# Optimization experiments

Measured on AMD Instinct MI355X. Metric: run time of the kernel, lower is better.

Reference implementation:

```python
import jax, jax.numpy as jnp
import numpy as np

EPS = 1e-5

def _offset_conv(x, w, b):
    # 3x3 conv, padding=1, producing 2*K*K offset channels (standard DeformConv2D v1)
    out = jax.lax.conv_general_dilated(x, w, (1, 1), ((1, 1), (1, 1)),
                                       dimension_numbers=('NCHW', 'OIHW', 'NCHW'))
    return out + b[None, :, None, None]

def _bilinear_gather(x, py, px):
    # x: [B,C,H,W]; py,px: [B,K2,H,W] float sample coords -> [B,C,K2,H,W]
    B, C, H, W = x.shape
    py = jnp.clip(py, 0.0, H - 1.0)
    px = jnp.clip(px, 0.0, W - 1.0)
    y0 = jnp.floor(py)
    x0 = jnp.floor(px)
    wy = py - y0
    wx = px - x0
    y0i = y0.astype(jnp.int32)
    x0i = x0.astype(jnp.int32)
    y1i = jnp.minimum(y0i + 1, H - 1)
    x1i = jnp.minimum(x0i + 1, W - 1)
    xf = x.reshape(B, C, H * W)
    K2, Ho, Wo = py.shape[1], py.shape[2], py.shape[3]
    def gather(yy, xx):
        idx = (yy * W + xx).reshape(B, 1, -1)  # broadcast over C
        return jnp.take_along_axis(xf, idx, axis=2).reshape(B, C, K2, Ho, Wo)
    v00 = gather(y0i, x0i)
    v01 = gather(y0i, x1i)
    v10 = gather(y1i, x0i)
    v11 = gather(y1i, x1i)
    wy = wy[:, None]
    wx = wx[:, None]
    return (v00 * (1 - wy) * (1 - wx) + v01 * (1 - wy) * wx
            + v10 * wy * (1 - wx) + v11 * wy * wx)

def _deform_dw(x, w_off, b_off, w_dw, k):
    # depthwise deformable conv, kernel k, padding k//2 (same spatial size)
    B, C, H, W = x.shape
    K2 = k * k
    off = _offset_conv(x, w_off, b_off)      # [B, 2*K2, H, W]
    dy, dx = off[:, :K2], off[:, K2:]
    r = (k - 1) // 2
    pn = jnp.arange(-r, r + 1, dtype=x.dtype)
    pn_y = jnp.repeat(pn, k)[None, :, None, None]  # [1,K2,1,1]
    pn_x = jnp.tile(pn, k)[None, :, None, None]
    gy = jnp.arange(H, dtype=x.dtype)[None, None, :, None]
    gx = jnp.arange(W, dtype=x.dtype)[None, None, None, :]
    py = gy + pn_y + dy
    px = gx + pn_x + dx
    samp = _bilinear_gather(x, py, px)        # [B,C,K2,H,W]
    return jnp.einsum('bckhw,ck->bchw', samp, w_dw.reshape(C, K2))

def _bn_relu(x, g, b, m, v):
    inv = g / jnp.sqrt(v + EPS)
    return jax.nn.relu(x * inv[None, :, None, None] + (b - m * inv)[None, :, None, None])

def setup_inputs() -> dict:
    key = jax.random.key(0)
    B, C, H, W, O = 4, 96, 64, 64, 192
    ks = jax.random.split(key, 32)
    d = {'x': jax.random.normal(ks[0], (B, C, H, W), jnp.float32)}
    i = 1
    for k in (3, 5, 7):
        K2 = k * k
        d[f'w_off{k}'] = 0.01 * jax.random.normal(ks[i], (2 * K2, C, 3, 3), jnp.float32); i += 1
        d[f'b_off{k}'] = jnp.zeros((2 * K2,), jnp.float32)
        d[f'w_dw{k}'] = jax.random.normal(ks[i], (C, k, k), jnp.float32) / k; i += 1
        d[f'g{k}'] = jnp.ones((C,), jnp.float32)
        d[f'be{k}'] = jnp.zeros((C,), jnp.float32)
        d[f'm{k}'] = 0.1 * jax.random.normal(ks[i], (C,), jnp.float32); i += 1
        d[f'v{k}'] = jax.random.uniform(ks[i], (C,), jnp.float32, 0.5, 1.5); i += 1
    d['w_pw'] = jax.random.normal(ks[i], (O, 3 * C), jnp.float32) / np.sqrt(3 * C).astype(np.float32); i += 1
    d['gp'] = jnp.ones((O,), jnp.float32)
    d['bp'] = jnp.zeros((O,), jnp.float32)
    d['mp'] = 0.1 * jax.random.normal(ks[i], (O,), jnp.float32); i += 1
    d['vp'] = jax.random.uniform(ks[i], (O,), jnp.float32, 0.5, 1.5)
    return d

def reference(x, w_off3, b_off3, w_dw3, g3, be3, m3, v3,
              w_off5, b_off5, w_dw5, g5, be5, m5, v5,
              w_off7, b_off7, w_dw7, g7, be7, m7, v7,
              w_pw, gp, bp, mp, vp):
    x1 = _bn_relu(_deform_dw(x, w_off3, b_off3, w_dw3, 3), g3, be3, m3, v3)
    x2 = _bn_relu(_deform_dw(x, w_off5, b_off5, w_dw5, 5), g5, be5, m5, v5)
    x3 = _bn_relu(_deform_dw(x, w_off7, b_off7, w_dw7, 7), g7, be7, m7, v7)
    xc = jnp.concatenate([x1, x2, x3], axis=1)  # [B, 3C, H, W]
    out = jnp.einsum('bchw,oc->bohw', xc, w_pw)  # 1x1 conv
    return _bn_relu(out, gp, bp, mp, vp)
```

## Files before the change

kernel.cpp:

```cpp
#include <hip/hip_runtime.h>
#include <hip/hip_fp16.h>
#include <math.h>

typedef unsigned short u16;
typedef _Float16 f16x8 __attribute__((ext_vector_type(8)));
typedef float f32x4 __attribute__((ext_vector_type(4)));

#define HWp 4096
#define Cc 96
#define Bb 4
#define Oo 192
#define C3 288

#define OFF_WDWT  0
#define OFF_BCAT  14112
#define OFF_SBR   14304
#define OFF_HBR   14592
#define OFF_SPW   14880
#define OFF_HPW   15072
#define FP32_END  15264
#define BF_XTPAD  0
#define BF_WOF    1672704
#define BF_WPW    1838592

__device__ __forceinline__ u16 f2h(float f) { return __half_as_ushort(__float2half(f)); }
__device__ __forceinline__ unsigned h2u(__half2 h) { union { __half2 h; unsigned u; } t; t.h = h; return t.u; }
__device__ __forceinline__ __half2 u2h(unsigned u) { union { __half2 h; unsigned u; } t; t.u = u; return t.h; }

#define PREP_N (165888 + 55296 + 14112 + 192 + 288 + 288 + 192 + 192 + 24960)
#define PREP_BLK ((PREP_N + 255) / 256)

__global__ __launch_bounds__(256) void prep_kernel(
    const float* __restrict__ x,
    const float* __restrict__ w3, const float* __restrict__ b3, const float* __restrict__ dw3,
    const float* __restrict__ g3, const float* __restrict__ be3, const float* __restrict__ m3, const float* __restrict__ v3,
    const float* __restrict__ w5, const float* __restrict__ b5, const float* __restrict__ dw5,
    const float* __restrict__ g5, const float* __restrict__ be5, const float* __restrict__ m5, const float* __restrict__ v5,
    const float* __restrict__ w7, const float* __restrict__ b7, const float* __restrict__ dw7,
    const float* __restrict__ g7, const float* __restrict__ be7, const float* __restrict__ m7, const float* __restrict__ v7,
    const float* __restrict__ wpw,
    const float* __restrict__ gp, const float* __restrict__ bp, const float* __restrict__ mp, const float* __restrict__ vp,
    float* __restrict__ ws)
{
    __shared__ u16 sT[64 * 104];
    u16* bf = (u16*)(ws + FP32_END);
    const int tid = threadIdx.x;

    if (blockIdx.x < 256) {
        const int b = blockIdx.x >> 6, h = blockIdx.x & 63;
        const float* xb = x + (((size_t)b * Cc) << 12) + (h << 6);
#pragma unroll
        for (int it = 0; it < 24; ++it) {
            int j = tid + it * 256;
            int c = j >> 6, p = j & 63;
            sT[p * 104 + c] = f2h(xb[((size_t)c << 12) + p]);
        }
        __syncthreads();
        u16* dst = bf + BF_XTPAD + ((size_t)(b * 66 + h + 1) * 66 + 1) * 96;
#pragma unroll
        for (int it = 0; it < 6; ++it) {
            int j = tid + it * 256;
            int pos = j / 24, c4 = j % 24;
            const u16* s = &sT[pos * 104 + c4 * 4];
            *(uint2*)(dst + pos * 96 + c4 * 4) = make_uint2(
                (unsigned)s[0] | ((unsigned)s[1] << 16),
                (unsigned)s[2] | ((unsigned)s[3] << 16));
        }
        return;
    }

    int i = (blockIdx.x - 256) * 256 + tid;
    if (i < 165888) {
        int f = i / 13824, r = i % 13824;
        int s = r >> 9, l = r & 511;
        int lane = l >> 3, j = l & 7;
        int o = f * 16 + (lane & 15);
        int k = s * 32 + (lane >> 4) * 8 + j;
        int tap = k / 96, c = k % 96;
        float v = 0.f;
        if (o < 18)       v = w3[o * 864 + c * 9 + tap];
        else if (o < 68)  v = w5[(o - 18) * 864 + c * 9 + tap];
        else if (o < 166) v = w7[(o - 68) * 864 + c * 9 + tap];
        bf[BF_WOF + i] = f2h(v);
        return;
    }
    int j = i - 165888;
    if (j < 55296) {
        int f = j / 4608, r = j % 4608;
        int s = r >> 9, l = r & 511;
        int lane = l >> 3, jj = l & 7;
        int o = f * 16 + (lane & 15);
        int k = s * 32 + (lane >> 4) * 8 + jj;
        bf[BF_WPW + j] = f2h(wpw[o * C3 + k]);
        return;
    }
    j -= 55296;
    if (j < 14112) {
        int ksel = j / 4704, rem = j % 4704;
        int t = rem / 96, c = rem % 96;
        int K2 = (ksel == 0) ? 9 : (ksel == 1) ? 25 : 49;
        const float* dw = (ksel == 0) ? dw3 : (ksel == 1) ? dw5 : dw7;
        ws[OFF_WDWT + j] = (t < K2) ? dw[c * K2 + t] : 0.f;
        return;
    }
    j -= 14112;
    if (j < 192) {
        float v = 0.f;
        if (j < 18)       v = b3[j];
        else if (j < 68)  v = b5[j - 18];
        else if (j < 166) v = b7[j - 68];
        ws[OFF_BCAT + j] = v;
        return;
    }
    j -= 192;
    if (j < C3) {
        int ks = j / Cc, c = j % Cc;
        const float* g = (ks == 0) ? g3 : (ks == 1) ? g5 : g7;
        const float* v = (ks == 0) ? v3 : (ks == 1) ? v5 : v7;
        ws[OFF_SBR + j] = g[c] / sqrtf(v[c] + 1e-5f);
        return;
    }
    j -= C3;
    if (j < C3) {
        int ks = j / Cc, c = j % Cc;
        const float* g = (ks == 0) ? g3 : (ks == 1) ? g5 : g7;
        const float* v = (ks == 0) ? v3 : (ks == 1) ? v5 : v7;
        const float* be = (ks == 0) ? be3 : (ks == 1) ? be5 : be7;
        const float* m = (ks == 0) ? m3 : (ks == 1) ? m5 : m7;
        float inv = g[c] / sqrtf(v[c] + 1e-5f);
        ws[OFF_HBR + j] = be[c] - m[c] * inv;
        return;
    }
    j -= C3;
    if (j < Oo) { ws[OFF_SPW + j] = gp[j] / sqrtf(vp[j] + 1e-5f); return; }
    j -= Oo;
    if (j < Oo) {
        float inv = gp[j] / sqrtf(vp[j] + 1e-5f);
        ws[OFF_HPW + j] = bp[j] - mp[j] * inv;
        return;
    }
    j -= Oo;
    if (j < 24960) {
        int c4 = j % 24, rem = j / 24;
        int cell = rem % 260, bb = rem / 260;
        int row, col;
        if (cell < 66)       { row = 0;  col = cell; }
        else if (cell < 132) { row = 65; col = cell - 66; }
        else if (cell < 196) { row = cell - 132 + 1; col = 0; }
        else                 { row = cell - 196 + 1; col = 65; }
        u16* dst = bf + BF_XTPAD + ((size_t)(bb * 66 + row) * 66 + col) * 96 + c4 * 4;
        *(uint2*)dst = make_uint2(0u, 0u);
        return;
    }
}

__global__ __launch_bounds__(256, 4) void mega_kernel(
    const float* __restrict__ ws, float* __restrict__ out)
{
    __shared__ uint4 regA[1328];
    __shared__ float regB[3072];
    u16* sX = (u16*)regA;
    uint4* sWI = regA;
    float* soff = regB;
    u16* ytile = (u16*)regB;

    const u16* bf = (const u16*)(ws + FP32_END);
    const u16* xp = bf + BF_XTPAD;
    const int tid = threadIdx.x;
    const int lane = tid & 63, wid = tid >> 6;
    const int lane15 = lane & 15, quad = lane >> 4;

    const int bx = blockIdx.x;
    const int xcd = bx & 7;
    const int b = xcd >> 1;
    const int tile = ((bx >> 3) << 1) + (xcd & 1);
    const int p0 = tile * 16;
    const int h = p0 >> 6;
    const int w0 = p0 & 63;

    {
        const u16* src = xp + ((size_t)(b * 66 + h) * 66 + w0) * 96;
        for (int j = tid; j < 1296; j += 256) {
            int r = j / 432;
            int rem = j % 432;
            int col = rem / 24, c4 = rem % 24;
            uint2 v = *(const uint2*)(src + ((size_t)(r * 66 + col)) * 96 + c4 * 4);
            *(uint2*)(&sX[(r * 18 + col) * 104 + c4 * 4]) = v;
        }
    }
    __syncthreads();

    {
        const u16* wof = bf + BF_WOF;
        f32x4 acc[3];
#pragma unroll
        for (int ff = 0; ff < 3; ++ff) acc[ff] = (f32x4){0.f, 0.f, 0.f, 0.f};
#pragma unroll
        for (int tap = 0; tap < 9; ++tap) {
            const int ky2 = tap / 3, kx2 = tap % 3;
            const u16* brow = &sX[(ky2 * 18 + kx2 + lane15) * 104 + quad * 8];
#pragma unroll
            for (int cc = 0; cc < 3; ++cc) {
                f16x8 bb = *(const f16x8*)(brow + cc * 32);
                const int s = tap * 3 + cc;
#pragma unroll
                for (int ff = 0; ff < 3; ++ff) {
                    const int f = wid * 3 + ff;
                    f16x8 a = *(const f16x8*)(wof + ((size_t)(f * 27 + s) * 64 + lane) * 8);
                    acc[ff] = __builtin_amdgcn_mfma_f32_16x16x32_f16(a, bb, acc[ff], 0, 0, 0);
                }
            }
        }
        const float* bcat = ws + OFF_BCAT;
#pragma unroll
        for (int ff = 0; ff < 3; ++ff) {
#pragma unroll
            for (int r = 0; r < 4; ++r) {
                int co = (wid * 3 + ff) * 16 + quad * 4 + r;
                soff[co * 16 + lane15] = acc[ff][r] + bcat[co];
            }
        }
    }
    __syncthreads();

    for (int i = tid; i < 1328; i += 256) {
        int gt = i >> 4, q = i & 15;
        int K, K2, R, tb, t;
        if (gt < 9)       { K = 3; K2 = 9;  R = 1; tb = 0;  t = gt; }
        else if (gt < 34) { K = 5; K2 = 25; R = 2; tb = 18; t = gt - 9; }
        else              { K = 7; K2 = 49; R = 3; tb = 68; t = gt - 34; }
        int ky = t / K - R, kx = t % K - R;
        float dy = soff[(tb + t) * 16 + q];
        float dx = soff[(tb + K2 + t) * 16 + q];
        float py = fminf(fmaxf((float)(h + ky) + dy, 0.f), 63.f);
        float px = fminf(fmaxf((float)(w0 + q + kx) + dx, 0.f), 63.f);
        float fy = floorf(py), fx = floorf(px);
        int y0 = (int)fy, x0 = (int)fx;
        float wy = py - fy, wx = px - fx;
        int y1 = min(y0 + 1, 63), x1 = min(x0 + 1, 63);
        float w11 = wy * wx;
        float w10 = wy - w11;
        float w01 = wx - w11;
        float w00 = 1.f - wy - wx + w11;
        unsigned wA = h2u(__floats2half2_rn(w00, w01));
        unsigned wB = h2u(__floats2half2_rn(w10, w11));
        unsigned o00 = (unsigned)((y0 + 1) * 66 + (x0 + 1)) * 192u;
        unsigned d01 = (unsigned)(x1 - x0) * 192u;
        unsigned d10 = (unsigned)(y1 - y0) * 12672u;
        sWI[i] = make_uint4(wA, wB, o00, d01 | (d10 << 16));
    }
    __syncthreads();

    if (tid < 192) {
        const int c8 = tid % 12;
        const int q  = tid / 12;
        const int c = c8 * 8;
        const u16* xh = xp + (size_t)b * 66 * 66 * 96;
        const char* xcb = (const char*)xh + c * 2;

#pragma unroll
        for (int seg = 0; seg < 3; ++seg) {
            const int g0 = (seg == 0) ? 0 : (seg == 1) ? 9 : 34;
            const int g1 = (seg == 0) ? 9 : (seg == 1) ? 34 : 83;
            const float* wdT = ws + OFF_WDWT + seg * 4704 + c;
            float acc[8];
#pragma unroll
            for (int k = 0; k < 8; ++k) acc[k] = 0.f;

            for (int gt = g0; gt < g1; ++gt) {
                const uint4 e = sWI[(gt << 4) + q];
                const __half2 wAh = u2h(e.x), wBh = u2h(e.y);
                const __half2 w00b = __low2half2(wAh), w01b = __high2half2(wAh);
                const __half2 w10b = __low2half2(wBh), w11b = __high2half2(wBh);
                const unsigned d01 = e.w & 0xffffu, d10 = e.w >> 16;
                const uint4 u00 = *(const uint4*)(xcb + e.z);
                const uint4 u01 = *(const uint4*)(xcb + e.z + d01);
                const uint4 u10 = *(const uint4*)(xcb + e.z + d10);
                const uint4 u11 = *(const uint4*)(xcb + e.z + d10 + d01);
                const float4 wda = *(const float4*)(wdT + (gt - g0) * 96);
                const float4 wdb = *(const float4*)(wdT + (gt - g0) * 96 + 4);
                const unsigned a00[4] = {u00.x, u00.y, u00.z, u00.w};
                const unsigned a01[4] = {u01.x, u01.y, u01.z, u01.w};
                const unsigned a10[4] = {u10.x, u10.y, u10.z, u10.w};
                const unsigned a11[4] = {u11.x, u11.y, u11.z, u11.w};
                const float wd[8] = {wda.x, wda.y, wda.z, wda.w, wdb.x, wdb.y, wdb.z, wdb.w};
#pragma unroll
                for (int d = 0; d < 4; ++d) {
                    __half2 v = __hmul2(w00b, u2h(a00[d]));
                    v = __hfma2(w01b, u2h(a01[d]), v);
                    v = __hfma2(w10b, u2h(a10[d]), v);
                    v = __hfma2(w11b, u2h(a11[d]), v);
                    acc[2 * d]     = fmaf(wd[2 * d],     __low2float(v),  acc[2 * d]);
                    acc[2 * d + 1] = fmaf(wd[2 * d + 1], __high2float(v), acc[2 * d + 1]);
                }
            }

            const int cb = seg * Cc + c;
            const float4 sa = *(const float4*)(ws + OFF_SBR + cb);
            const float4 sb = *(const float4*)(ws + OFF_SBR + cb + 4);
            const float4 ha = *(const float4*)(ws + OFF_HBR + cb);
            const float4 hb = *(const float4*)(ws + OFF_HBR + cb + 4);
            const float ss[8] = {sa.x, sa.y, sa.z, sa.w, sb.x, sb.y, sb.z, sb.w};
            const float hh8[8] = {ha.x, ha.y, ha.z, ha.w, hb.x, hb.y, hb.z, hb.w};
            unsigned rr[4];
#pragma unroll
            for (int d = 0; d < 4; ++d) {
                float lo = fmaxf(fmaf(acc[2 * d],     ss[2 * d],     hh8[2 * d]),     0.f);
                float hi = fmaxf(fmaf(acc[2 * d + 1], ss[2 * d + 1], hh8[2 * d + 1]), 0.f);
                rr[d] = h2u(__floats2half2_rn(lo, hi));
            }
            *(uint4*)(ytile + q * 296 + cb) = make_uint4(rr[0], rr[1], rr[2], rr[3]);
        }
    }
    __syncthreads();

    {
        const u16* wpw = bf + BF_WPW;
        f32x4 acc[3];
#pragma unroll
        for (int ff = 0; ff < 3; ++ff) acc[ff] = (f32x4){0.f, 0.f, 0.f, 0.f};
        const u16* brow = &ytile[lane15 * 296 + quad * 8];
#pragma unroll
        for (int s = 0; s < 9; ++s) {
            f16x8 bb = *(const f16x8*)(brow + s * 32);
#pragma unroll
            for (int ff = 0; ff < 3; ++ff) {
                const int f = wid * 3 + ff;
                f16x8 a = *(const f16x8*)(wpw + ((size_t)(f * 9 + s) * 64 + lane) * 8);
                acc[ff] = __builtin_amdgcn_mfma_f32_16x16x32_f16(a, bb, acc[ff], 0, 0, 0);
            }
        }
        const float* spw = ws + OFF_SPW;
        const float* hpw = ws + OFF_HPW;
        const int p = p0 + lane15;
#pragma unroll
        for (int ff = 0; ff < 3; ++ff) {
#pragma unroll
            for (int r = 0; r < 4; ++r) {
                int o = (wid * 3 + ff) * 16 + quad * 4 + r;
                out[(((size_t)(b * Oo + o)) << 12) + p] =
                    fmaxf(fmaf(acc[ff][r], spw[o], hpw[o]), 0.f);
            }
        }
    }
}

extern "C" void kernel_launch(void* const* d_in, const int* in_sizes, int n_in,
                              void* d_out, int out_size, void* d_ws, size_t ws_size,
                              hipStream_t stream)
{
    const float* x     = (const float*)d_in[0];
    const float* w3    = (const float*)d_in[1];
    const float* b3    = (const float*)d_in[2];
    const float* dw3   = (const float*)d_in[3];
    const float* g3    = (const float*)d_in[4];
    const float* be3   = (const float*)d_in[5];
    const float* m3    = (const float*)d_in[6];
    const float* v3    = (const float*)d_in[7];
    const float* w5    = (const float*)d_in[8];
    const float* b5    = (const float*)d_in[9];
    const float* dw5   = (const float*)d_in[10];
    const float* g5    = (const float*)d_in[11];
    const float* be5   = (const float*)d_in[12];
    const float* m5    = (const float*)d_in[13];
    const float* v5    = (const float*)d_in[14];
    const float* w7    = (const float*)d_in[15];
    const float* b7    = (const float*)d_in[16];
    const float* dw7   = (const float*)d_in[17];
    const float* g7    = (const float*)d_in[18];
    const float* be7   = (const float*)d_in[19];
    const float* m7    = (const float*)d_in[20];
    const float* v7    = (const float*)d_in[21];
    const float* wpw   = (const float*)d_in[22];
    const float* gp    = (const float*)d_in[23];
    const float* bp    = (const float*)d_in[24];
    const float* mp    = (const float*)d_in[25];
    const float* vp    = (const float*)d_in[26];

    float* ws = (float*)d_ws;
    float* out = (float*)d_out;

    {
        prep_kernel<<<256 + PREP_BLK, 256, 0, stream>>>(
            x,
            w3, b3, dw3, g3, be3, m3, v3,
            w5, b5, dw5, g5, be5, m5, v5,
            w7, b7, dw7, g7, be7, m7, v7,
            wpw, gp, bp, mp, vp, ws);
    }
    {
        mega_kernel<<<1024, 256, 0, stream>>>(ws, out);
    }
}
```

Before: 174.5 us.

## Spread deformable sampling over all threads with 6 channels each and software prefetch

The bilinear gather stage now uses every thread in the block (16 channel groups of 6 channels × q positions) instead of only the first 192 threads with 8 channels each. The tap loop is restructured into a two-stage software pipeline that issues the next tap's gathers and weights before consuming the current ones. The aim is more active lanes and latency hiding on the scattered global loads. In exchange, 12-byte loads are less aligned than 16-byte ones and the double-buffered registers raise register pressure.

```diff
diff --git a/kernel.cpp b/kernel.cpp
--- a/kernel.cpp
+++ b/kernel.cpp
@@ -251,10 +251,10 @@
     }
     __syncthreads();
 
-    if (tid < 192) {
-        const int c8 = tid % 12;
-        const int q  = tid / 12;
-        const int c = c8 * 8;
+    {
+        const int g6 = tid & 15;
+        const int q  = tid >> 4;
+        const int c  = g6 * 6;
         const u16* xh = xp + (size_t)b * 66 * 66 * 96;
         const char* xcb = (const char*)xh + c * 2;
 
@@ -263,53 +263,80 @@
             const int g0 = (seg == 0) ? 0 : (seg == 1) ? 9 : 34;
             const int g1 = (seg == 0) ? 9 : (seg == 1) ? 34 : 83;
             const float* wdT = ws + OFF_WDWT + seg * 4704 + c;
-            float acc[8];
-#pragma unroll
-            for (int k = 0; k < 8; ++k) acc[k] = 0.f;
-
-            for (int gt = g0; gt < g1; ++gt) {
-                const uint4 e = sWI[(gt << 4) + q];
-                const __half2 wAh = u2h(e.x), wBh = u2h(e.y);
-                const __half2 w00b = __low2half2(wAh), w01b = __high2half2(wAh);
-                const __half2 w10b = __low2half2(wBh), w11b = __high2half2(wBh);
-                const unsigned d01 = e.w & 0xffffu, d10 = e.w >> 16;
-                const uint4 u00 = *(const uint4*)(xcb + e.z);
-                const uint4 u01 = *(const uint4*)(xcb + e.z + d01);
-                const uint4 u10 = *(const uint4*)(xcb + e.z + d10);
-                const uint4 u11 = *(const uint4*)(xcb + e.z + d10 + d01);
-                const float4 wda = *(const float4*)(wdT + (gt - g0) * 96);
-                const float4 wdb = *(const float4*)(wdT + (gt - g0) * 96 + 4);
-                const unsigned a00[4] = {u00.x, u00.y, u00.z, u00.w};
-                const unsigned a01[4] = {u01.x, u01.y, u01.z, u01.w};
-                const unsigned a10[4] = {u10.x, u10.y, u10.z, u10.w};
-                const unsigned a11[4] = {u11.x, u11.y, u11.z, u11.w};
-                const float wd[8] = {wda.x, wda.y, wda.z, wda.w, wdb.x, wdb.y, wdb.z, wdb.w};
-#pragma unroll
-                for (int d = 0; d < 4; ++d) {
-                    __half2 v = __hmul2(w00b, u2h(a00[d]));
-                    v = __hfma2(w01b, u2h(a01[d]), v);
-                    v = __hfma2(w10b, u2h(a10[d]), v);
-                    v = __hfma2(w11b, u2h(a11[d]), v);
-                    acc[2 * d]     = fmaf(wd[2 * d],     __low2float(v),  acc[2 * d]);
-                    acc[2 * d + 1] = fmaf(wd[2 * d + 1], __high2float(v), acc[2 * d + 1]);
-                }
+            float acc0 = 0.f, acc1 = 0.f, acc2 = 0.f,
+                  acc3 = 0.f, acc4 = 0.f, acc5 = 0.f;
+
+            uint3 u00A, u01A, u10A, u11A, u00B, u01B, u10B, u11B;
+            float2 wd0A, wd1A, wd2A, wd0B, wd1B, wd2B;
+            unsigned hAA, hBA, hAB, hBB;
+
+#define PREF(U00,U01,U10,U11,WD0,WD1,WD2,HA,HB,GT) { \
+            const uint4 e = sWI[((GT) << 4) + q]; \
+            HA = e.x; HB = e.y; \
+            const unsigned d01 = e.w & 0xffffu, d10 = e.w >> 16; \
+            const char* pb = xcb + e.z; \
+            U00 = *(const uint3*)(pb); \
+            U01 = *(const uint3*)(pb + d01); \
+            U10 = *(const uint3*)(pb + d10); \
+            U11 = *(const uint3*)(pb + d10 + d01); \
+            const float* wrow = wdT + ((GT) - g0) * 96; \
+            WD0 = *(const float2*)(wrow); \
+            WD1 = *(const float2*)(wrow + 2); \
+            WD2 = *(const float2*)(wrow + 4); }
+
+#define CONS(U00,U01,U10,U11,WD0,WD1,WD2,HA,HB) { \
+            const __half2 wAh = u2h(HA), wBh = u2h(HB); \
+            const __half2 w00b = __low2half2(wAh), w01b = __high2half2(wAh); \
+            const __half2 w10b = __low2half2(wBh), w11b = __high2half2(wBh); \
+            __half2 v; \
+            v = __hmul2(w00b, u2h(U00.x)); v = __hfma2(w01b, u2h(U01.x), v); \
+            v = __hfma2(w10b, u2h(U10.x), v); v = __hfma2(w11b, u2h(U11.x), v); \
+            acc0 = fmaf(WD0.x, __low2float(v),  acc0); \
+            acc1 = fmaf(WD0.y, __high2float(v), acc1); \
+            v = __hmul2(w00b, u2h(U00.y)); v = __hfma2(w01b, u2h(U01.y), v); \
+            v = __hfma2(w10b, u2h(U10.y), v); v = __hfma2(w11b, u2h(U11.y), v); \
+            acc2 = fmaf(WD1.x, __low2float(v),  acc2); \
+            acc3 = fmaf(WD1.y, __high2float(v), acc3); \
+            v = __hmul2(w00b, u2h(U00.z)); v = __hfma2(w01b, u2h(U01.z), v); \
+            v = __hfma2(w10b, u2h(U10.z), v); v = __hfma2(w11b, u2h(U11.z), v); \
+            acc4 = fmaf(WD2.x, __low2float(v),  acc4); \
+            acc5 = fmaf(WD2.y, __high2float(v), acc5); }
+
+            PREF(u00A,u01A,u10A,u11A,wd0A,wd1A,wd2A,hAA,hBA, g0);
+            int gt = g0;
+#pragma unroll 1
+            while (gt + 1 < g1) {
+                PREF(u00B,u01B,u10B,u11B,wd0B,wd1B,wd2B,hAB,hBB, gt + 1);
+                CONS(u00A,u01A,u10A,u11A,wd0A,wd1A,wd2A,hAA,hBA);
+                ++gt;
+                if (gt + 1 < g1)
+                    PREF(u00A,u01A,u10A,u11A,wd0A,wd1A,wd2A,hAA,hBA, gt + 1);
+                CONS(u00B,u01B,u10B,u11B,wd0B,wd1B,wd2B,hAB,hBB);
+                ++gt;
             }
+            if (gt < g1)
+                CONS(u00A,u01A,u10A,u11A,wd0A,wd1A,wd2A,hAA,hBA);
+#undef PREF
+#undef CONS
 
             const int cb = seg * Cc + c;
-            const float4 sa = *(const float4*)(ws + OFF_SBR + cb);
-            const float4 sb = *(const float4*)(ws + OFF_SBR + cb + 4);
-            const float4 ha = *(const float4*)(ws + OFF_HBR + cb);
-            const float4 hb = *(const float4*)(ws + OFF_HBR + cb + 4);
-            const float ss[8] = {sa.x, sa.y, sa.z, sa.w, sb.x, sb.y, sb.z, sb.w};
-            const float hh8[8] = {ha.x, ha.y, ha.z, ha.w, hb.x, hb.y, hb.z, hb.w};
-            unsigned rr[4];
-#pragma unroll
-            for (int d = 0; d < 4; ++d) {
-                float lo = fmaxf(fmaf(acc[2 * d],     ss[2 * d],     hh8[2 * d]),     0.f);
-                float hi = fmaxf(fmaf(acc[2 * d + 1], ss[2 * d + 1], hh8[2 * d + 1]), 0.f);
-                rr[d] = h2u(__floats2half2_rn(lo, hi));
-            }
-            *(uint4*)(ytile + q * 296 + cb) = make_uint4(rr[0], rr[1], rr[2], rr[3]);
+            const float2 s0 = *(const float2*)(ws + OFF_SBR + cb);
+            const float2 s1 = *(const float2*)(ws + OFF_SBR + cb + 2);
+            const float2 s2 = *(const float2*)(ws + OFF_SBR + cb + 4);
+            const float2 h0 = *(const float2*)(ws + OFF_HBR + cb);
+            const float2 h1 = *(const float2*)(ws + OFF_HBR + cb + 2);
+            const float2 h2 = *(const float2*)(ws + OFF_HBR + cb + 4);
+            unsigned r0 = h2u(__floats2half2_rn(
+                fmaxf(fmaf(acc0, s0.x, h0.x), 0.f),
+                fmaxf(fmaf(acc1, s0.y, h0.y), 0.f)));
+            unsigned r1 = h2u(__floats2half2_rn(
+                fmaxf(fmaf(acc2, s1.x, h1.x), 0.f),
+                fmaxf(fmaf(acc3, s1.y, h1.y), 0.f)));
+            unsigned r2 = h2u(__floats2half2_rn(
+                fmaxf(fmaf(acc4, s2.x, h2.x), 0.f),
+                fmaxf(fmaf(acc5, s2.y, h2.y), 0.f)));
+            unsigned* yt = (unsigned*)(ytile + q * 296 + cb);
+            yt[0] = r0; yt[1] = r1; yt[2] = r2;
         }
     }
     __syncthreads();
```

After: 189.6 us. 1.09x slower.
